# Performance work log

Hardware: AMD Instinct MI355X
Metric: run time of the kernel (lower is better)

The kernel has to match this reference:

```python
import jax, jax.numpy as jnp
import numpy as np

N = 128  # n_hidden == n_inputs == n_outputs
TWO_PI = 2.0 * np.pi


def build_unitary(mzi_phases, output_phases):
    """Clements mesh: n layers of disjoint 2x2 MZI rotations, composed left-to-right.
    Within a layer the MZIs act on disjoint pairs, so their product equals one dense
    layer matrix (matches the sequential torch loop exactly)."""
    n = N
    U = jnp.eye(n, dtype=jnp.complex64)
    idx = 0
    for layer in range(n):
        pi = np.arange(layer % 2, n - 1, 2)  # left indices of pairs this layer
        m = len(pi)
        theta = mzi_phases[idx:idx + 2 * m:2]
        phi = mzi_phases[idx + 1:idx + 2 * m:2]
        idx += 2 * m
        ct = jnp.cos(theta).astype(jnp.complex64)
        st = jnp.sin(theta).astype(jnp.complex64)
        ep = jnp.exp(1j * phi.astype(jnp.complex64))
        L = jnp.eye(n, dtype=jnp.complex64)
        L = L.at[pi, pi].set(ct * ep)
        L = L.at[pi, pi + 1].set(st)
        L = L.at[pi + 1, pi].set(st)
        L = L.at[pi + 1, pi + 1].set(-ct * jnp.conj(ep))
        U = U @ L
    return U * jnp.exp(1j * output_phases.astype(jnp.complex64))[None, :]


def nofu(z, alpha, beta):
    eps = 1e-8
    intensity = jnp.abs(z) ** 2 + eps
    a = jnp.clip(alpha, 0.0, 10.0)
    b = jnp.clip(beta, 0.0, 10.0)
    transmission = jnp.exp(-a[None, :] / (1.0 + b[None, :] * intensity))
    return z * jnp.sqrt(transmission).astype(z.dtype)


def setup_inputs() -> dict:
    key = jax.random.key(0)
    ks = jax.random.split(key, 16)
    B = 65536
    num_mzi_phases = N * (N - 1)  # 2 phases per MZI
    inp = {
        "x": jax.random.normal(ks[0], (B, N), jnp.float32),
        "input_phases": jnp.zeros((N,), jnp.float32),
        "mzi_phases1": jax.random.uniform(ks[1], (num_mzi_phases,), jnp.float32) * TWO_PI,
        "out_phases1": jnp.zeros((N,), jnp.float32),
        "alpha1": jnp.full((N,), 0.5, jnp.float32),
        "beta1": jnp.full((N,), 0.2, jnp.float32),
        "mzi_phases2": jax.random.uniform(ks[2], (num_mzi_phases,), jnp.float32) * TWO_PI,
        "out_phases2": jnp.zeros((N,), jnp.float32),
        "alpha2": jnp.full((N,), 0.5, jnp.float32),
        "beta2": jnp.full((N,), 0.2, jnp.float32),
        "mzi_phases3": jax.random.uniform(ks[3], (num_mzi_phases,), jnp.float32) * TWO_PI,
        "out_phases3": jnp.zeros((N,), jnp.float32),
        "W": jax.random.normal(ks[4], (N, 2 * N), jnp.float32) * 0.05,  # torch Linear weight [out,in]
        "b": jnp.zeros((N,), jnp.float32),
    }
    return inp


def reference(x, input_phases, mzi_phases1, out_phases1, alpha1, beta1,
              mzi_phases2, out_phases2, alpha2, beta2,
              mzi_phases3, out_phases3, W, b):
    # Eval mode: no BatchNorm, no dropout.
    z = x.astype(jnp.complex64) * jnp.exp(1j * input_phases.astype(jnp.complex64))[None, :]
    z = z @ build_unitary(mzi_phases1, out_phases1)
    z = nofu(z, alpha1, beta1)
    z = z @ build_unitary(mzi_phases2, out_phases2)
    z = nofu(z, alpha2, beta2)
    z = z @ build_unitary(mzi_phases3, out_phases3)
    real_output = jnp.concatenate([jnp.real(z), jnp.imag(z)], axis=1)
    return real_output @ W.T + b[None, :]
```

## Files before the change

kernel.cpp:

```cpp
#include <hip/hip_runtime.h>
#include <math.h>

typedef __attribute__((ext_vector_type(8))) short bf16x8;
typedef __attribute__((ext_vector_type(4))) float f32x4;
typedef unsigned short u16;

__device__ __forceinline__ unsigned short f2bf(float f) {
    unsigned u = __builtin_bit_cast(unsigned, f);
    u += 0x7fffu + ((u >> 16) & 1u);
    return (unsigned short)(u >> 16);
}

__global__ __launch_bounds__(128) void prep_trig_kernel(
    const float* __restrict__ mzi1, const float* __restrict__ mzi2,
    const float* __restrict__ mzi3, const float* __restrict__ W,
    float4* __restrict__ trig, u16* __restrict__ P4)
{
    const int b = blockIdx.x, t = threadIdx.x;
    if (b < 384) {
        if (t >= 64) return;
        const int s = b >> 7, L = b & 127;
        const float* mzi = (s == 0) ? mzi1 : ((s == 1) ? mzi2 : mzi3);
        const int start = L & 1;
        const int m = (128 - start) >> 1;
        float4 v = make_float4(1.f, 0.f, 1.f, 0.f);
        if (t < m) {
            const int off = (L >> 1) * 254 + start * 128 + 2 * t;
            float th = mzi[off], ph = mzi[off + 1];
            float st, ct, sp, cp;
            __sincosf(th, &st, &ct);
            __sincosf(ph, &sp, &cp);
            v = make_float4(ct, st, cp, sp);
        }
        trig[b * 64 + t] = v;
    } else {
        const int n = b - 384;
        const int j = t;
        const int rre = ((j >> 4) * 32) + (j & 15);
        P4[n * 256 + rre]      = f2bf(W[n * 256 + j]);
        P4[n * 256 + rre + 16] = f2bf(W[n * 256 + j + 128]);
    }
}

__global__ __launch_bounds__(64) void build_pack_kernel(
    const float* __restrict__ inph,
    const float* __restrict__ outph1, const float* __restrict__ outph2,
    const float* __restrict__ outph3,
    const float4* __restrict__ trig,
    u16* __restrict__ P1, u16* __restrict__ P2, u16* __restrict__ P3)
{
    const int s = blockIdx.x >> 7, r = blockIdx.x & 127, t = threadIdx.x;
    const float4* tg = trig + s * 128 * 64;

    float2 a = make_float2(0.f, 0.f), b2 = make_float2(0.f, 0.f);
    if (s == 0) {
        float sp, cp; __sincosf(inph[r], &sp, &cp);
        if (2 * t == r)     a  = make_float2(cp, sp);
        if (2 * t + 1 == r) b2 = make_float2(cp, sp);
    } else {
        if (2 * t == r)     a.x  = 1.f;
        if (2 * t + 1 == r) b2.x = 1.f;
    }

    float4 tv[4];
    #pragma unroll
    for (int i = 0; i < 4; ++i) tv[i] = tg[i * 64 + t];

    #pragma unroll 4
    for (int L = 0; L < 128; ++L) {
        const float4 c = tv[L & 3];
        if (L < 124) tv[L & 3] = tg[(L + 4) * 64 + t];
        if ((L & 1) == 0) {
            float pr = c.x * (a.x * c.z - a.y * c.w) + c.y * b2.x;
            float pi = c.x * (a.x * c.w + a.y * c.z) + c.y * b2.y;
            float qr = c.y * a.x - c.x * (b2.x * c.z + b2.y * c.w);
            float qi = c.y * a.y - c.x * (b2.y * c.z - b2.x * c.w);
            a = make_float2(pr, pi); b2 = make_float2(qr, qi);
        } else {
            float2 an;
            an.x = __shfl_down(a.x, 1); an.y = __shfl_down(a.y, 1);
            float pr = c.x * (b2.x * c.z - b2.y * c.w) + c.y * an.x;
            float pi = c.x * (b2.x * c.w + b2.y * c.z) + c.y * an.y;
            float qr = c.y * b2.x - c.x * (an.x * c.z + an.y * c.w);
            float qi = c.y * b2.y - c.x * (an.y * c.z - an.x * c.w);
            if (t < 63) b2 = make_float2(pr, pi);
            float2 qs;
            qs.x = __shfl_up(qr, 1); qs.y = __shfl_up(qi, 1);
            if (t >= 1) a = qs;
        }
    }

    const float* outph = (s == 0) ? outph1 : ((s == 1) ? outph2 : outph3);
    #pragma unroll
    for (int h = 0; h < 2; ++h) {
        const int j = 2 * t + h;
        float2 w = h ? b2 : a;
        float sp, cp; __sincosf(outph[j], &sp, &cp);
        const float wr = w.x * cp - w.y * sp;
        const float wi = w.x * sp + w.y * cp;
        const int cre = ((j >> 4) * 32) + (j & 15);
        if (s == 0) {
            P1[cre * 128 + r]        = f2bf(wr);
            P1[(cre + 16) * 128 + r] = f2bf(wi);
        } else {
            u16* P = (s == 1) ? P2 : P3;
            const int rre = ((r >> 4) * 32) + (r & 15);
            P[cre * 256 + rre]             = f2bf(wr);
            P[cre * 256 + rre + 16]        = f2bf(-wi);
            P[(cre + 16) * 256 + rre]      = f2bf(wi);
            P[(cre + 16) * 256 + rre + 16] = f2bf(wr);
        }
    }
}

__global__ __launch_bounds__(512, 4) void ficonn_mfma_kernel(
    const float* __restrict__ x,
    const u16* __restrict__ P1, const u16* __restrict__ P2,
    const u16* __restrict__ P3, const u16* __restrict__ P4,
    const float* __restrict__ al1, const float* __restrict__ be1,
    const float* __restrict__ al2, const float* __restrict__ be2,
    const float* __restrict__ bias, float* __restrict__ out)
{
    __shared__ __align__(16) char zBuf[2][32768];
    char* const z0 = zBuf[0];
    char* const z1 = zBuf[1];

    const int tid  = threadIdx.x;
    const int lane = tid & 63;
    const int wv   = tid >> 6;
    const int l16  = lane & 15;
    const int kg   = lane >> 4;
    const int nb   = wv * 32;
    const size_t rowBase = (size_t)blockIdx.x * 64;

    const int jf = wv * 16 + l16;
    const float av1 = 0.5f * fminf(fmaxf(al1[jf], 0.f), 10.f);
    const float bv1 = fminf(fmaxf(be1[jf], 0.f), 10.f);
    const float av2 = 0.5f * fminf(fmaxf(al2[jf], 0.f), 10.f);
    const float bv2 = fminf(fmaxf(be2[jf], 0.f), 10.f);

    {
        const float4* xg = (const float4*)(x + rowBase * 128);
        #pragma unroll
        for (int i = 0; i < 4; ++i) {
            const int idx = tid + i * 512;
            const int row = idx >> 5;
            const int c4  = idx & 31;
            float4 f = xg[idx];
            uint2 v;
            v.x = (unsigned)f2bf(f.x) | ((unsigned)f2bf(f.y) << 16);
            v.y = (unsigned)f2bf(f.z) | ((unsigned)f2bf(f.w) << 16);
            const unsigned byte = ((unsigned)(row * 512 + c4 * 8)) ^ ((unsigned)(row & 31) << 4);
            *(uint2*)(z0 + byte) = v;
        }
    }
    __syncthreads();

    f32x4 acc[4][2];

    #pragma unroll
    for (int mt = 0; mt < 4; ++mt)
        #pragma unroll
        for (int nt = 0; nt < 2; ++nt) acc[mt][nt] = (f32x4){0.f, 0.f, 0.f, 0.f};

    #pragma unroll 2
    for (int ksl = 0; ksl < 4; ++ksl) {
        const int k0 = ksl * 32 + kg * 8;
        bf16x8 A[4];
        #pragma unroll
        for (int mt = 0; mt < 4; ++mt) {
            const int row = mt * 16 + l16;
            const unsigned byte = ((unsigned)(row * 512 + k0 * 2)) ^ ((unsigned)(row & 31) << 4);
            A[mt] = *(const bf16x8*)(z0 + byte);
        }
        #pragma unroll
        for (int nt = 0; nt < 2; ++nt) {
            bf16x8 Bf = *(const bf16x8*)&P1[(nb + nt * 16 + l16) * 128 + k0];
            #pragma unroll
            for (int mt = 0; mt < 4; ++mt)
                acc[mt][nt] = __builtin_amdgcn_mfma_f32_16x16x32_bf16(A[mt], Bf, acc[mt][nt], 0, 0, 0);
        }
    }

    #pragma unroll
    for (int mt = 0; mt < 4; ++mt)
        #pragma unroll
        for (int r = 0; r < 4; ++r) {
            float re = acc[mt][0][r], im = acc[mt][1][r];
            float I = fmaf(re, re, fmaf(im, im, 1e-8f));
            float fct = __expf(-av1 / fmaf(bv1, I, 1.f));
            re *= fct; im *= fct;
            const int row = mt * 16 + kg * 4 + r;
            const int colRe = nb + l16;
            const unsigned sw = (unsigned)(row & 31) << 4;
            *(u16*)(z1 + (((unsigned)(row * 512 + colRe * 2)) ^ sw)) = f2bf(re);
            *(u16*)(z1 + (((unsigned)(row * 512 + (colRe + 16) * 2)) ^ sw)) = f2bf(im);
        }
    __syncthreads();

    #pragma unroll
    for (int mt = 0; mt < 4; ++mt)
        #pragma unroll
        for (int nt = 0; nt < 2; ++nt) acc[mt][nt] = (f32x4){0.f, 0.f, 0.f, 0.f};

    #pragma unroll 2
    for (int ks = 0; ks < 8; ++ks) {
        const int k0 = ks * 32 + kg * 8;
        bf16x8 A[4];
        #pragma unroll
        for (int mt = 0; mt < 4; ++mt) {
            const int row = mt * 16 + l16;
            const unsigned byte = ((unsigned)(row * 512 + k0 * 2)) ^ ((unsigned)(row & 31) << 4);
            A[mt] = *(const bf16x8*)(z1 + byte);
        }
        #pragma unroll
        for (int nt = 0; nt < 2; ++nt) {
            bf16x8 Bf = *(const bf16x8*)&P2[(nb + nt * 16 + l16) * 256 + k0];
            #pragma unroll
            for (int mt = 0; mt < 4; ++mt)
                acc[mt][nt] = __builtin_amdgcn_mfma_f32_16x16x32_bf16(A[mt], Bf, acc[mt][nt], 0, 0, 0);
        }
    }

    #pragma unroll
    for (int mt = 0; mt < 4; ++mt)
        #pragma unroll
        for (int r = 0; r < 4; ++r) {
            float re = acc[mt][0][r], im = acc[mt][1][r];
            float I = fmaf(re, re, fmaf(im, im, 1e-8f));
            float fct = __expf(-av2 / fmaf(bv2, I, 1.f));
            re *= fct; im *= fct;
            const int row = mt * 16 + kg * 4 + r;
            const int colRe = nb + l16;
            const unsigned sw = (unsigned)(row & 31) << 4;
            *(u16*)(z0 + (((unsigned)(row * 512 + colRe * 2)) ^ sw)) = f2bf(re);
            *(u16*)(z0 + (((unsigned)(row * 512 + (colRe + 16) * 2)) ^ sw)) = f2bf(im);
        }
    __syncthreads();

    #pragma unroll
    for (int mt = 0; mt < 4; ++mt)
        #pragma unroll
        for (int nt = 0; nt < 2; ++nt) acc[mt][nt] = (f32x4){0.f, 0.f, 0.f, 0.f};

    #pragma unroll 2
    for (int ks = 0; ks < 8; ++ks) {
        const int k0 = ks * 32 + kg * 8;
        bf16x8 A[4];
        #pragma unroll
        for (int mt = 0; mt < 4; ++mt) {
            const int row = mt * 16 + l16;
            const unsigned byte = ((unsigned)(row * 512 + k0 * 2)) ^ ((unsigned)(row & 31) << 4);
            A[mt] = *(const bf16x8*)(z0 + byte);
        }
        #pragma unroll
        for (int nt = 0; nt < 2; ++nt) {
            bf16x8 Bf = *(const bf16x8*)&P3[(nb + nt * 16 + l16) * 256 + k0];
            #pragma unroll
            for (int mt = 0; mt < 4; ++mt)
                acc[mt][nt] = __builtin_amdgcn_mfma_f32_16x16x32_bf16(A[mt], Bf, acc[mt][nt], 0, 0, 0);
        }
    }

    #pragma unroll
    for (int mt = 0; mt < 4; ++mt)
        #pragma unroll
        for (int r = 0; r < 4; ++r) {
            const int row = mt * 16 + kg * 4 + r;
            const int colRe = nb + l16;
            const unsigned sw = (unsigned)(row & 31) << 4;
            *(u16*)(z1 + (((unsigned)(row * 512 + colRe * 2)) ^ sw)) = f2bf(acc[mt][0][r]);
            *(u16*)(z1 + (((unsigned)(row * 512 + (colRe + 16) * 2)) ^ sw)) = f2bf(acc[mt][1][r]);
        }
    __syncthreads();

    f32x4 facc[4];
    #pragma unroll
    for (int mt = 0; mt < 4; ++mt) facc[mt] = (f32x4){0.f, 0.f, 0.f, 0.f};

    const int nb2 = wv * 16;
    #pragma unroll 2
    for (int ks = 0; ks < 8; ++ks) {
        const int k0 = ks * 32 + kg * 8;
        bf16x8 A[4];
        #pragma unroll
        for (int mt = 0; mt < 4; ++mt) {
            const int row = mt * 16 + l16;
            const unsigned byte = ((unsigned)(row * 512 + k0 * 2)) ^ ((unsigned)(row & 31) << 4);
            A[mt] = *(const bf16x8*)(z1 + byte);
        }
        bf16x8 Bf = *(const bf16x8*)&P4[(nb2 + l16) * 256 + k0];
        #pragma unroll
        for (int mt = 0; mt < 4; ++mt)
            facc[mt] = __builtin_amdgcn_mfma_f32_16x16x32_bf16(A[mt], Bf, facc[mt], 0, 0, 0);
    }

    const float bcol = bias[nb2 + l16];
    #pragma unroll
    for (int mt = 0; mt < 4; ++mt)
        #pragma unroll
        for (int r = 0; r < 4; ++r) {
            const size_t row = rowBase + mt * 16 + kg * 4 + r;
            out[row * 128 + nb2 + l16] = facc[mt][r] + bcol;
        }
}

extern "C" void kernel_launch(void* const* d_in, const int* in_sizes, int n_in,
                              void* d_out, int out_size, void* d_ws, size_t ws_size,
                              hipStream_t stream)
{
    const float* x      = (const float*)d_in[0];
    const float* inph   = (const float*)d_in[1];
    const float* mzi1   = (const float*)d_in[2];
    const float* outph1 = (const float*)d_in[3];
    const float* alpha1 = (const float*)d_in[4];
    const float* beta1  = (const float*)d_in[5];
    const float* mzi2   = (const float*)d_in[6];
    const float* outph2 = (const float*)d_in[7];
    const float* alpha2 = (const float*)d_in[8];
    const float* beta2  = (const float*)d_in[9];
    const float* mzi3   = (const float*)d_in[10];
    const float* outph3 = (const float*)d_in[11];
    const float* W      = (const float*)d_in[12];
    const float* bias   = (const float*)d_in[13];

    const int B = in_sizes[0] / 128;

    float4* trig = (float4*)d_ws;
    u16* P1 = (u16*)((char*)d_ws + 393216);
    u16* P2 = P1 + 32768;
    u16* P3 = P2 + 65536;
    u16* P4 = P3 + 65536;

    prep_trig_kernel<<<512, 128, 0, stream>>>(mzi1, mzi2, mzi3, W, trig, P4);
    build_pack_kernel<<<384, 64, 0, stream>>>(inph, outph1, outph2, outph3, trig, P1, P2, P3);
    ficonn_mfma_kernel<<<B / 64, 512, 0, stream>>>(
        x, P1, P2, P3, P4, alpha1, beta1, alpha2, beta2, bias, (float*)d_out);
}
```

Baseline: 86.23 us.

## Fuse trig prep into unitary build and halve main kernel row tile

Merges the trig-precompute and unitary-build kernels into one launch. The build loop now loads raw MZI phases and computes sincos inline instead of reading a precomputed trig buffer from global memory. Separately, the main MFMA kernel processes 32 rows per block instead of 64, which halves LDS use and lets launch bounds ask for 8 blocks per CU. This trades one kernel launch and a global round-trip for redundant sincos work (each of 128 blocks per stage recomputes it). The smaller tile also means each block reloads the P matrices from global/L2 for half as many rows, which raises weight traffic.

```diff
diff --git a/kernel.cpp b/kernel.cpp
--- a/kernel.cpp
+++ b/kernel.cpp
@@ -11,46 +11,28 @@
     return (unsigned short)(u >> 16);
 }
 
-__global__ __launch_bounds__(128) void prep_trig_kernel(
+__global__ __launch_bounds__(128) void prep_all_kernel(
     const float* __restrict__ mzi1, const float* __restrict__ mzi2,
-    const float* __restrict__ mzi3, const float* __restrict__ W,
-    float4* __restrict__ trig, u16* __restrict__ P4)
+    const float* __restrict__ mzi3, const float* __restrict__ inph,
+    const float* __restrict__ outph1, const float* __restrict__ outph2,
+    const float* __restrict__ outph3, const float* __restrict__ W,
+    u16* __restrict__ P1, u16* __restrict__ P2, u16* __restrict__ P3,
+    u16* __restrict__ P4)
 {
     const int b = blockIdx.x, t = threadIdx.x;
-    if (b < 384) {
-        if (t >= 64) return;
-        const int s = b >> 7, L = b & 127;
-        const float* mzi = (s == 0) ? mzi1 : ((s == 1) ? mzi2 : mzi3);
-        const int start = L & 1;
-        const int m = (128 - start) >> 1;
-        float4 v = make_float4(1.f, 0.f, 1.f, 0.f);
-        if (t < m) {
-            const int off = (L >> 1) * 254 + start * 128 + 2 * t;
-            float th = mzi[off], ph = mzi[off + 1];
-            float st, ct, sp, cp;
-            __sincosf(th, &st, &ct);
-            __sincosf(ph, &sp, &cp);
-            v = make_float4(ct, st, cp, sp);
-        }
-        trig[b * 64 + t] = v;
-    } else {
+
+    if (b >= 384) {
         const int n = b - 384;
         const int j = t;
         const int rre = ((j >> 4) * 32) + (j & 15);
         P4[n * 256 + rre]      = f2bf(W[n * 256 + j]);
         P4[n * 256 + rre + 16] = f2bf(W[n * 256 + j + 128]);
-    }
-}
-
-__global__ __launch_bounds__(64) void build_pack_kernel(
-    const float* __restrict__ inph,
-    const float* __restrict__ outph1, const float* __restrict__ outph2,
-    const float* __restrict__ outph3,
-    const float4* __restrict__ trig,
-    u16* __restrict__ P1, u16* __restrict__ P2, u16* __restrict__ P3)
-{
-    const int s = blockIdx.x >> 7, r = blockIdx.x & 127, t = threadIdx.x;
-    const float4* tg = trig + s * 128 * 64;
+        return;
+    }
+    if (t >= 64) return;
+
+    const int s = b >> 7, r = b & 127;
+    const float* mzi = (s == 0) ? mzi1 : ((s == 1) ? mzi2 : mzi3);
 
     float2 a = make_float2(0.f, 0.f), b2 = make_float2(0.f, 0.f);
     if (s == 0) {
@@ -62,27 +44,39 @@
         if (2 * t + 1 == r) b2.x = 1.f;
     }
 
-    float4 tv[4];
-    #pragma unroll
-    for (int i = 0; i < 4; ++i) tv[i] = tg[i * 64 + t];
+    auto ldmz = [&](int L) -> float2 {
+        const int start = L & 1;
+        const int m = 64 - start;
+        if (t < m) {
+            const int off = (L >> 1) * 254 + start * 128 + 2 * t;
+            return *(const float2*)(mzi + off);
+        }
+        return make_float2(0.f, 0.f);
+    };
+    float2 mz[4];
+    #pragma unroll
+    for (int i = 0; i < 4; ++i) mz[i] = ldmz(i);
 
     #pragma unroll 4
     for (int L = 0; L < 128; ++L) {
-        const float4 c = tv[L & 3];
-        if (L < 124) tv[L & 3] = tg[(L + 4) * 64 + t];
+        const float2 v = mz[L & 3];
+        if (L < 124) mz[L & 3] = ldmz(L + 4);
+        float st, ct, sp, cp;
+        __sincosf(v.x, &st, &ct);
+        __sincosf(v.y, &sp, &cp);
         if ((L & 1) == 0) {
-            float pr = c.x * (a.x * c.z - a.y * c.w) + c.y * b2.x;
-            float pi = c.x * (a.x * c.w + a.y * c.z) + c.y * b2.y;
-            float qr = c.y * a.x - c.x * (b2.x * c.z + b2.y * c.w);
-            float qi = c.y * a.y - c.x * (b2.y * c.z - b2.x * c.w);
+            float pr = ct * (a.x * cp - a.y * sp) + st * b2.x;
+            float pi = ct * (a.x * sp + a.y * cp) + st * b2.y;
+            float qr = st * a.x - ct * (b2.x * cp + b2.y * sp);
+            float qi = st * a.y - ct * (b2.y * cp - b2.x * sp);
             a = make_float2(pr, pi); b2 = make_float2(qr, qi);
         } else {
             float2 an;
             an.x = __shfl_down(a.x, 1); an.y = __shfl_down(a.y, 1);
-            float pr = c.x * (b2.x * c.z - b2.y * c.w) + c.y * an.x;
-            float pi = c.x * (b2.x * c.w + b2.y * c.z) + c.y * an.y;
-            float qr = c.y * b2.x - c.x * (an.x * c.z + an.y * c.w);
-            float qi = c.y * b2.y - c.x * (an.y * c.z - an.x * c.w);
+            float pr = ct * (b2.x * cp - b2.y * sp) + st * an.x;
+            float pi = ct * (b2.x * sp + b2.y * cp) + st * an.y;
+            float qr = st * b2.x - ct * (an.x * cp + an.y * sp);
+            float qi = st * b2.y - ct * (an.y * cp - an.x * sp);
             if (t < 63) b2 = make_float2(pr, pi);
             float2 qs;
             qs.x = __shfl_up(qr, 1); qs.y = __shfl_up(qi, 1);
@@ -113,7 +107,7 @@
     }
 }
 
-__global__ __launch_bounds__(512, 4) void ficonn_mfma_kernel(
+__global__ __launch_bounds__(512, 8) void ficonn_mfma_kernel(
     const float* __restrict__ x,
     const u16* __restrict__ P1, const u16* __restrict__ P2,
     const u16* __restrict__ P3, const u16* __restrict__ P4,
@@ -121,7 +115,7 @@
     const float* __restrict__ al2, const float* __restrict__ be2,
     const float* __restrict__ bias, float* __restrict__ out)
 {
-    __shared__ __align__(16) char zBuf[2][32768];
+    __shared__ __align__(16) char zBuf[2][16384];
     char* const z0 = zBuf[0];
     char* const z1 = zBuf[1];
 
@@ -131,7 +125,7 @@
     const int l16  = lane & 15;
     const int kg   = lane >> 4;
     const int nb   = wv * 32;
-    const size_t rowBase = (size_t)blockIdx.x * 64;
+    const size_t rowBase = (size_t)blockIdx.x * 32;
 
     const int jf = wv * 16 + l16;
     const float av1 = 0.5f * fminf(fmaxf(al1[jf], 0.f), 10.f);
@@ -142,7 +136,7 @@
     {
         const float4* xg = (const float4*)(x + rowBase * 128);
         #pragma unroll
-        for (int i = 0; i < 4; ++i) {
+        for (int i = 0; i < 2; ++i) {
             const int idx = tid + i * 512;
             const int row = idx >> 5;
             const int c4  = idx & 31;
@@ -156,19 +150,19 @@
     }
     __syncthreads();
 
-    f32x4 acc[4][2];
-
-    #pragma unroll
-    for (int mt = 0; mt < 4; ++mt)
+    f32x4 acc[2][2];
+
+    #pragma unroll
+    for (int mt = 0; mt < 2; ++mt)
         #pragma unroll
         for (int nt = 0; nt < 2; ++nt) acc[mt][nt] = (f32x4){0.f, 0.f, 0.f, 0.f};
 
     #pragma unroll 2
     for (int ksl = 0; ksl < 4; ++ksl) {
         const int k0 = ksl * 32 + kg * 8;
-        bf16x8 A[4];
-        #pragma unroll
-        for (int mt = 0; mt < 4; ++mt) {
+        bf16x8 A[2];
+        #pragma unroll
+        for (int mt = 0; mt < 2; ++mt) {
             const int row = mt * 16 + l16;
             const unsigned byte = ((unsigned)(row * 512 + k0 * 2)) ^ ((unsigned)(row & 31) << 4);
             A[mt] = *(const bf16x8*)(z0 + byte);
@@ -177,13 +171,13 @@
         for (int nt = 0; nt < 2; ++nt) {
             bf16x8 Bf = *(const bf16x8*)&P1[(nb + nt * 16 + l16) * 128 + k0];
             #pragma unroll
-            for (int mt = 0; mt < 4; ++mt)
+            for (int mt = 0; mt < 2; ++mt)
                 acc[mt][nt] = __builtin_amdgcn_mfma_f32_16x16x32_bf16(A[mt], Bf, acc[mt][nt], 0, 0, 0);
         }
     }
 
     #pragma unroll
-    for (int mt = 0; mt < 4; ++mt)
+    for (int mt = 0; mt < 2; ++mt)
         #pragma unroll
         for (int r = 0; r < 4; ++r) {
             float re = acc[mt][0][r], im = acc[mt][1][r];
@@ -199,16 +193,16 @@
     __syncthreads();
 
     #pragma unroll
-    for (int mt = 0; mt < 4; ++mt)
+    for (int mt = 0; mt < 2; ++mt)
         #pragma unroll
         for (int nt = 0; nt < 2; ++nt) acc[mt][nt] = (f32x4){0.f, 0.f, 0.f, 0.f};
 
     #pragma unroll 2
     for (int ks = 0; ks < 8; ++ks) {
         const int k0 = ks * 32 + kg * 8;
-        bf16x8 A[4];
-        #pragma unroll
-        for (int mt = 0; mt < 4; ++mt) {
+        bf16x8 A[2];
+        #pragma unroll
+        for (int mt = 0; mt < 2; ++mt) {
             const int row = mt * 16 + l16;
             const unsigned byte = ((unsigned)(row * 512 + k0 * 2)) ^ ((unsigned)(row & 31) << 4);
             A[mt] = *(const bf16x8*)(z1 + byte);
@@ -217,13 +211,13 @@
         for (int nt = 0; nt < 2; ++nt) {
             bf16x8 Bf = *(const bf16x8*)&P2[(nb + nt * 16 + l16) * 256 + k0];
             #pragma unroll
-            for (int mt = 0; mt < 4; ++mt)
+            for (int mt = 0; mt < 2; ++mt)
                 acc[mt][nt] = __builtin_amdgcn_mfma_f32_16x16x32_bf16(A[mt], Bf, acc[mt][nt], 0, 0, 0);
         }
     }
 
     #pragma unroll
-    for (int mt = 0; mt < 4; ++mt)
+    for (int mt = 0; mt < 2; ++mt)
         #pragma unroll
         for (int r = 0; r < 4; ++r) {
             float re = acc[mt][0][r], im = acc[mt][1][r];
@@ -239,16 +233,16 @@
     __syncthreads();
 
     #pragma unroll
-    for (int mt = 0; mt < 4; ++mt)
+    for (int mt = 0; mt < 2; ++mt)
         #pragma unroll
         for (int nt = 0; nt < 2; ++nt) acc[mt][nt] = (f32x4){0.f, 0.f, 0.f, 0.f};
 
     #pragma unroll 2
     for (int ks = 0; ks < 8; ++ks) {
         const int k0 = ks * 32 + kg * 8;
-        bf16x8 A[4];
-        #pragma unroll
-        for (int mt = 0; mt < 4; ++mt) {
+        bf16x8 A[2];
+        #pragma unroll
+        for (int mt = 0; mt < 2; ++mt) {
             const int row = mt * 16 + l16;
             const unsigned byte = ((unsigned)(row * 512 + k0 * 2)) ^ ((unsigned)(row & 31) << 4);
             A[mt] = *(const bf16x8*)(z0 + byte);
@@ -257,13 +251,13 @@
         for (int nt = 0; nt < 2; ++nt) {
             bf16x8 Bf = *(const bf16x8*)&P3[(nb + nt * 16 + l16) * 256 + k0];
             #pragma unroll
-            for (int mt = 0; mt < 4; ++mt)
+            for (int mt = 0; mt < 2; ++mt)
                 acc[mt][nt] = __builtin_amdgcn_mfma_f32_16x16x32_bf16(A[mt], Bf, acc[mt][nt], 0, 0, 0);
         }
     }
 
     #pragma unroll
-    for (int mt = 0; mt < 4; ++mt)
+    for (int mt = 0; mt < 2; ++mt)
         #pragma unroll
         for (int r = 0; r < 4; ++r) {
             const int row = mt * 16 + kg * 4 + r;
@@ -274,30 +268,30 @@
         }
     __syncthreads();
 
-    f32x4 facc[4];
-    #pragma unroll
-    for (int mt = 0; mt < 4; ++mt) facc[mt] = (f32x4){0.f, 0.f, 0.f, 0.f};
+    f32x4 facc[2];
+    #pragma unroll
+    for (int mt = 0; mt < 2; ++mt) facc[mt] = (f32x4){0.f, 0.f, 0.f, 0.f};
 
     const int nb2 = wv * 16;
     #pragma unroll 2
     for (int ks = 0; ks < 8; ++ks) {
         const int k0 = ks * 32 + kg * 8;
-        bf16x8 A[4];
-        #pragma unroll
-        for (int mt = 0; mt < 4; ++mt) {
+        bf16x8 A[2];
+        #pragma unroll
+        for (int mt = 0; mt < 2; ++mt) {
             const int row = mt * 16 + l16;
             const unsigned byte = ((unsigned)(row * 512 + k0 * 2)) ^ ((unsigned)(row & 31) << 4);
             A[mt] = *(const bf16x8*)(z1 + byte);
         }
         bf16x8 Bf = *(const bf16x8*)&P4[(nb2 + l16) * 256 + k0];
         #pragma unroll
-        for (int mt = 0; mt < 4; ++mt)
+        for (int mt = 0; mt < 2; ++mt)
             facc[mt] = __builtin_amdgcn_mfma_f32_16x16x32_bf16(A[mt], Bf, facc[mt], 0, 0, 0);
     }
 
     const float bcol = bias[nb2 + l16];
     #pragma unroll
-    for (int mt = 0; mt < 4; ++mt)
+    for (int mt = 0; mt < 2; ++mt)
         #pragma unroll
         for (int r = 0; r < 4; ++r) {
             const size_t row = rowBase + mt * 16 + kg * 4 + r;
@@ -326,14 +320,13 @@
 
     const int B = in_sizes[0] / 128;
 
-    float4* trig = (float4*)d_ws;
-    u16* P1 = (u16*)((char*)d_ws + 393216);
+    u16* P1 = (u16*)d_ws;
     u16* P2 = P1 + 32768;
     u16* P3 = P2 + 65536;
     u16* P4 = P3 + 65536;
 
-    prep_trig_kernel<<<512, 128, 0, stream>>>(mzi1, mzi2, mzi3, W, trig, P4);
-    build_pack_kernel<<<384, 64, 0, stream>>>(inph, outph1, outph2, outph3, trig, P1, P2, P3);
-    ficonn_mfma_kernel<<<B / 64, 512, 0, stream>>>(
+    prep_all_kernel<<<512, 128, 0, stream>>>(
+        mzi1, mzi2, mzi3, inph, outph1, outph2, outph3, W, P1, P2, P3, P4);
+    ficonn_mfma_kernel<<<B / 32, 512, 0, stream>>>(
         x, P1, P2, P3, P4, alpha1, beta1, alpha2, beta2, bias, (float*)d_out);
 }
```

Result: slower. 122.7 us (+42.3%).
